# Kernel tuning notes

Measured on AMD Instinct MI355X. Metric: run time of the kernel, lower is better.

The kernel has to match this reference:

```python
import jax, jax.numpy as jnp
import numpy as np

N, E, T, D, C = 20000, 160000, 3, 128, 128  # nodes, edges, replicas, in=out feat dim, num_classes
NUM_EDGES = 128  # linear1 output width (must be <= C for the H scatter to be in-range)


def setup_inputs() -> dict:
    key = jax.random.key(0)
    ks = jax.random.split(key, 8)
    s = 1.0 / np.sqrt(D)
    return {
        "edge_index": jax.random.randint(ks[0], (2, E), 0, N, dtype=jnp.int32),
        "features": jax.random.normal(ks[1], (N, D), jnp.float32),
        "lin_W": jax.random.normal(ks[2], (T, D, D), jnp.float32) * s,   # t per-replica Linears
        "lin_b": jnp.zeros((T, D), jnp.float32),
        "gcn1_W": jax.random.normal(ks[3], (D, C), jnp.float32) * s,
        "gcn1_b": jnp.zeros((C,), jnp.float32),
        "gcn2_W": jax.random.normal(ks[4], (C, C), jnp.float32) * s,
        "gcn2_b": jnp.zeros((C,), jnp.float32),
        "lin1_W": jax.random.normal(ks[5], (C, NUM_EDGES), jnp.float32) * s,
        "lin1_b": jnp.zeros((NUM_EDGES,), jnp.float32),
    }


def _gcn(x, W, b, src, dst, n):
    """PyG GCNConv: add self-loops, symmetric deg^-1/2 normalization, scatter-add."""
    loop = jnp.arange(n, dtype=src.dtype)
    src = jnp.concatenate([src, loop])
    dst = jnp.concatenate([dst, loop])
    deg = jax.ops.segment_sum(jnp.ones(src.shape, x.dtype), dst, num_segments=n)
    dinv = jax.lax.rsqrt(deg)  # deg >= 1 because of self-loops
    norm = dinv[src] * dinv[dst]
    xw = x @ W
    return jax.ops.segment_sum(xw[src] * norm[:, None], dst, num_segments=n) + b


def reference(edge_index, features, lin_W, lin_b, gcn1_W, gcn1_b, gcn2_W, gcn2_b, lin1_W, lin1_b):
    src, dst = edge_index[0], edge_index[1]
    n = features.shape[0]
    t = lin_W.shape[0]
    scale = features.shape[1] ** -0.5  # out_features ** -0.5
    # t linear replicas, concatenated along nodes -> [t*n, D]
    transformed = (jnp.einsum('nd,tde->tne', features, lin_W) + lin_b[:, None, :]).reshape(t * n, -1)
    # replicate-selection via cosine similarity (exact torch index order:
    # src.repeat_interleave(t) vs dst.repeat(t))
    rep_src = jnp.repeat(src, t)
    exp_dst = jnp.tile(dst, t)
    a = features[rep_src]
    bb = transformed[exp_dst]
    sim = (a * bb).sum(-1) / jnp.maximum(
        jnp.linalg.norm(a, axis=-1) * jnp.linalg.norm(bb, axis=-1), 1e-8)
    best = jnp.argmax(sim.reshape(-1, t), axis=1)            # [E]
    best_nodes = dst + best.astype(dst.dtype) * n            # index into replica blocks
    # extra edges: (arange(n), arange(n) + i*n) for i in range(t)
    extra_src = jnp.tile(jnp.arange(n, dtype=src.dtype), t)
    extra_dst = (jnp.arange(n, dtype=src.dtype)[None, :]
                 + (jnp.arange(t, dtype=src.dtype) * n)[:, None]).reshape(-1)
    src_all = jnp.concatenate([src, src, extra_src])
    dst_all = jnp.concatenate([dst, best_nodes, extra_dst])
    nt = (t + 1) * n
    all_features = jnp.concatenate([features, transformed], axis=0)  # [(t+1)n, D]
    # GCN backbone (dropout = identity in eval mode)
    h = jax.nn.relu(all_features)
    h = jax.nn.relu(_gcn(h, gcn1_W, gcn1_b, src_all, dst_all, nt))
    all_features2 = _gcn(h, gcn2_W, gcn2_b, src_all, dst_all, nt)    # [(t+1)n, C]
    logits = jax.nn.relu(all_features2) @ lin1_W + lin1_b            # [(t+1)n, NUM_EDGES]
    num_classes = gcn2_b.shape[0]
    classes = jnp.argmax(logits.reshape(t + 1, n, -1), axis=-1)      # [t+1, n]
    H = jax.nn.one_hot(classes, num_classes, dtype=features.dtype).sum(0)  # [n, C] vote counts
    # per-class segment sum over nodes with H[:, j] > 0 (only first n rows are ever selected)
    mask = (H > 0).astype(features.dtype)                            # [n, C]
    hyperedge_features = mask.T @ all_features2[:n]                  # [C, D]
    dots = (all_features @ hyperedge_features.T) * scale             # [(t+1)n, C]
    H = jax.nn.softmax(H, axis=0)
    return H, hyperedge_features, dots
```

## Files before the change

kernel.cpp:

```cpp
#include <hip/hip_runtime.h>
#include <math.h>

#define NN 20000
#define NE 160000
#define TT 3
#define DD 128
#define NTOT 80000
#define N3 60000
#define NBLK1 79
#define SIMW 20000

__device__ __forceinline__ float waveReduceSum(float v) {
#pragma unroll
  for (int off = 32; off >= 1; off >>= 1)
    v += __shfl_xor(v, off, 64);
  return v;
}

__device__ __forceinline__ void atomAddF(float* p, float v) {
  unsafeAtomicAdd(p, v);
}

__global__ __launch_bounds__(256) void k_copy_feat(const float* __restrict__ src,
                                                   float* __restrict__ dst, int n4) {
  int i = blockIdx.x * 256 + threadIdx.x;
  if (i < n4) ((float4*)dst)[i] = ((const float4*)src)[i];
}

template <int RELU_IN, int TRANS_W, int DO_ARGMAX>
__global__ __launch_bounds__(512, 3) void gemm128(const float* __restrict__ X,
                                                  const float* __restrict__ W,
                                                  const float* __restrict__ bias,
                                                  float* __restrict__ out, int M,
                                                  float scale, int wStride, int bStride,
                                                  long oStride, int* __restrict__ cls) {
  __shared__ float Ws[128 * 132];
  const int tid = threadIdx.x;
  const int rbase = blockIdx.x * 160;
  W += (long)blockIdx.y * wStride;
  if (bias) bias += (long)blockIdx.y * bStride;
  out += (long)blockIdx.y * oStride;

#pragma unroll
  for (int it = 0; it < 8; ++it) {
    int idx = (tid + it * 512) * 4;
    int kl = idx >> 7, c = idx & 127;
    float4 w;
    if (!TRANS_W) {
      w = *(const float4*)&W[kl * 128 + c];
    } else {
      w.x = W[(c + 0) * 128 + kl];
      w.y = W[(c + 1) * 128 + kl];
      w.z = W[(c + 2) * 128 + kl];
      w.w = W[(c + 3) * 128 + kl];
    }
    *(float4*)&Ws[kl * 132 + c] = w;
  }

  const int tc = tid & 15, tr = tid >> 4;
  const int c0a = tc * 4, c0b = 64 + tc * 4;
  const int r0 = tr * 5;

  const float4* xrow[5];
#pragma unroll
  for (int i = 0; i < 5; ++i) {
    int gr = rbase + r0 + i;
    int gc = (gr < M) ? gr : 0;
    xrow[i] = (const float4*)(X + (long)gc * 128);
  }

  float acc[5][8];
#pragma unroll
  for (int i = 0; i < 5; ++i)
#pragma unroll
    for (int j = 0; j < 8; ++j) acc[i][j] = 0.f;

  float4 xc[5], xn[5];
#pragma unroll
  for (int i = 0; i < 5; ++i) {
    float4 v = xrow[i][0];
    if (RELU_IN) {
      v.x = fmaxf(v.x, 0.f);
      v.y = fmaxf(v.y, 0.f);
      v.z = fmaxf(v.z, 0.f);
      v.w = fmaxf(v.w, 0.f);
    }
    xc[i] = v;
  }

  __syncthreads();

  for (int kq = 0; kq < 32; ++kq) {
    if (kq < 31) {
#pragma unroll
      for (int i = 0; i < 5; ++i) {
        float4 v = xrow[i][kq + 1];
        if (RELU_IN) {
          v.x = fmaxf(v.x, 0.f);
          v.y = fmaxf(v.y, 0.f);
          v.z = fmaxf(v.z, 0.f);
          v.w = fmaxf(v.w, 0.f);
        }
        xn[i] = v;
      }
    }
    const int klb = kq * 4;
#pragma unroll
    for (int k = 0; k < 4; ++k) {
      const int kl = klb + k;
      const float4 wa = *(const float4*)&Ws[kl * 132 + c0a];
      const float4 wb = *(const float4*)&Ws[kl * 132 + c0b];
      float av[5];
#pragma unroll
      for (int i = 0; i < 5; ++i)
        av[i] = (k == 0) ? xc[i].x : (k == 1) ? xc[i].y : (k == 2) ? xc[i].z : xc[i].w;
      const float bv[8] = {wa.x, wa.y, wa.z, wa.w, wb.x, wb.y, wb.z, wb.w};
#pragma unroll
      for (int i = 0; i < 5; ++i)
#pragma unroll
        for (int j = 0; j < 8; ++j) acc[i][j] = fmaf(av[i], bv[j], acc[i][j]);
    }
    if (kq < 31) {
#pragma unroll
      for (int i = 0; i < 5; ++i) xc[i] = xn[i];
    }
  }

  float bb[8];
#pragma unroll
  for (int j = 0; j < 8; ++j) bb[j] = 0.f;
  if (bias) {
#pragma unroll
    for (int j = 0; j < 4; ++j) bb[j] = bias[c0a + j];
#pragma unroll
    for (int j = 0; j < 4; ++j) bb[4 + j] = bias[c0b + j];
  }

  if (DO_ARGMAX) {
#pragma unroll
    for (int i = 0; i < 5; ++i) {
      float bv = acc[i][0] * scale + bb[0];
      int bc = c0a;
#pragma unroll
      for (int j = 1; j < 8; ++j) {
        float v = acc[i][j] * scale + bb[j];
        int col = (j < 4) ? (c0a + j) : (c0b + j - 4);
        if (v > bv) {
          bv = v;
          bc = col;
        }
      }
#pragma unroll
      for (int off = 1; off <= 8; off <<= 1) {
        float ov = __shfl_xor(bv, off, 64);
        int oc = __shfl_xor(bc, off, 64);
        if (ov > bv || (ov == bv && oc < bc)) {
          bv = ov;
          bc = oc;
        }
      }
      int gr = rbase + r0 + i;
      if (tc == 0 && gr < M) cls[gr] = bc;
    }
  } else {
#pragma unroll
    for (int i = 0; i < 5; ++i) {
      int gr = rbase + r0 + i;
      if (gr < M) {
        float4 v0, v1;
        v0.x = acc[i][0] * scale + bb[0];
        v0.y = acc[i][1] * scale + bb[1];
        v0.z = acc[i][2] * scale + bb[2];
        v0.w = acc[i][3] * scale + bb[3];
        v1.x = acc[i][4] * scale + bb[4];
        v1.y = acc[i][5] * scale + bb[5];
        v1.z = acc[i][6] * scale + bb[6];
        v1.w = acc[i][7] * scale + bb[7];
        *(float4*)&out[(long)gr * 128 + c0a] = v0;
        *(float4*)&out[(long)gr * 128 + c0b] = v1;
      }
    }
  }
}

__global__ __launch_bounds__(256) void k_norms(const float* __restrict__ feat,
                                               const float* __restrict__ A,
                                               float* __restrict__ nf,
                                               float* __restrict__ nt0) {
  int w = blockIdx.x * 4 + (threadIdx.x >> 6);
  int lane = threadIdx.x & 63;
  if (w >= 2 * NN) return;
  const float* p = (w < NN) ? (feat + (long)w * 128) : (A + (long)(NN + (w - NN)) * 128);
  float2 v = *(const float2*)(p + lane * 2);
  float s = waveReduceSum(v.x * v.x + v.y * v.y);
  if (lane == 0) {
    float r = sqrtf(s);
    if (w < NN) nf[w] = r;
    else nt0[w - NN] = r;
  }
}

__global__ __launch_bounds__(256) void k_sim(const int* __restrict__ ei,
                                             const float* __restrict__ feat,
                                             const float* __restrict__ A,
                                             const float* __restrict__ nf,
                                             const float* __restrict__ nt0,
                                             int* __restrict__ bn) {
  const int t = threadIdx.x;
  const int lane = t & 31;
  const int half = (t >> 5) & 1;
  const int w = blockIdx.x * 4 + (t >> 6);

#define SIM_LOAD(I, E, DE, AV, B0, B1, B2, NA, NB0, NB1, NB2)              \
  {                                                                        \
    E = 2 * (w + (I)*SIMW) + half;                                         \
    DE = ei[NE + E];                                                       \
    int s_ = ei[E];                                                        \
    int j0_ = 3 * E;                                                       \
    if (j0_ >= NE) j0_ -= NE;                                              \
    if (j0_ >= NE) j0_ -= NE;                                              \
    int j1_ = j0_ + 1;                                                     \
    if (j1_ >= NE) j1_ -= NE;                                              \
    int j2_ = j0_ + 2;                                                     \
    if (j2_ >= NE) j2_ -= NE;                                              \
    int d0_ = ei[NE + j0_], d1_ = ei[NE + j1_], d2_ = ei[NE + j2_];        \
    AV = ((const float4*)(feat + (long)s_ * 128))[lane];                   \
    B0 = ((const float4*)(A + (long)(NN + d0_) * 128))[lane];              \
    B1 = ((const float4*)(A + (long)(NN + d1_) * 128))[lane];              \
    B2 = ((const float4*)(A + (long)(NN + d2_) * 128))[lane];              \
    NA = nf[s_];                                                           \
    NB0 = nt0[d0_];                                                        \
    NB1 = nt0[d1_];                                                        \
    NB2 = nt0[d2_];                                                        \
  }

  int ec, dec;
  float4 ac, b0c, b1c, b2c;
  float nac, nb0c, nb1c, nb2c;
  SIM_LOAD(0, ec, dec, ac, b0c, b1c, b2c, nac, nb0c, nb1c, nb2c);

#pragma unroll
  for (int i = 0; i < 4; ++i) {
    int en = 0, den = 0;
    float4 an, b0n, b1n, b2n;
    float nan2 = 0.f, nb0n = 0.f, nb1n = 0.f, nb2n = 0.f;
    if (i < 3) {
      SIM_LOAD(i + 1, en, den, an, b0n, b1n, b2n, nan2, nb0n, nb1n, nb2n);
    }
    float p0 = ac.x * b0c.x + ac.y * b0c.y + ac.z * b0c.z + ac.w * b0c.w;
    float p1 = ac.x * b1c.x + ac.y * b1c.y + ac.z * b1c.z + ac.w * b1c.w;
    float p2 = ac.x * b2c.x + ac.y * b2c.y + ac.z * b2c.z + ac.w * b2c.w;
#pragma unroll
    for (int off = 1; off <= 16; off <<= 1) {
      p0 += __shfl_xor(p0, off, 64);
      p1 += __shfl_xor(p1, off, 64);
      p2 += __shfl_xor(p2, off, 64);
    }
    float s0 = p0 / fmaxf(nac * nb0c, 1e-8f);
    float s1 = p1 / fmaxf(nac * nb1c, 1e-8f);
    float s2 = p2 / fmaxf(nac * nb2c, 1e-8f);
    int bk = 0;
    float bv = s0;
    if (s1 > bv) {
      bv = s1;
      bk = 1;
    }
    if (s2 > bv) {
      bv = s2;
      bk = 2;
    }
    if (lane == 0) bn[ec] = dec + bk * NN;
    if (i < 3) {
      ec = en;
      dec = den;
      ac = an;
      b0c = b0n;
      b1c = b1n;
      b2c = b2n;
      nac = nan2;
      nb0c = nb0n;
      nb1c = nb1n;
      nb2c = nb2n;
    }
  }
#undef SIM_LOAD
}

__global__ __launch_bounds__(256) void k_zero_count(int* __restrict__ count) {
  int v = blockIdx.x * 256 + threadIdx.x;
  if (v < NTOT) count[v] = 0;
}

__global__ __launch_bounds__(256) void k_count(const int* __restrict__ ei,
                                               const int* __restrict__ bn,
                                               int* __restrict__ count) {
  int e = blockIdx.x * 256 + threadIdx.x;
  if (e < NE) {
    atomicAdd(&count[ei[NE + e]], 1);
    atomicAdd(&count[bn[e]], 1);
  }
}

__global__ __launch_bounds__(256) void k_dinv(const int* __restrict__ count,
                                              float* __restrict__ dinv) {
  int v = blockIdx.x * 256 + threadIdx.x;
  if (v < NTOT) {
    float deg = (float)count[v] + ((v < N3) ? 2.f : 1.f);
    dinv[v] = 1.f / sqrtf(deg);
  }
}

__global__ __launch_bounds__(256) void k_scan1(const int* __restrict__ count,
                                               int* __restrict__ start,
                                               int* __restrict__ bsum) {
  __shared__ int sh[256];
  const int b = blockIdx.x, t = threadIdx.x;
  const int base = b * 1024 + t * 4;
  int c[4];
  int s = 0;
#pragma unroll
  for (int k = 0; k < 4; ++k) {
    int idx = base + k;
    c[k] = (idx < NTOT) ? count[idx] : 0;
    s += c[k];
  }
  sh[t] = s;
  __syncthreads();
  for (int off = 1; off < 256; off <<= 1) {
    int v = (t >= off) ? sh[t - off] : 0;
    __syncthreads();
    sh[t] += v;
    __syncthreads();
  }
  if (t == 255) bsum[b] = sh[255];
  int run = sh[t] - s;
#pragma unroll
  for (int k = 0; k < 4; ++k) {
    int idx = base + k;
    if (idx < NTOT) start[idx] = run;
    run += c[k];
  }
}

__global__ __launch_bounds__(256) void k_scan2(int* __restrict__ bsum) {
  __shared__ int sh[256];
  const int t = threadIdx.x;
  int v = (t < NBLK1) ? bsum[t] : 0;
  sh[t] = v;
  __syncthreads();
  for (int off = 1; off < 256; off <<= 1) {
    int u = (t >= off) ? sh[t - off] : 0;
    __syncthreads();
    sh[t] += u;
    __syncthreads();
  }
  if (t < NBLK1) bsum[t] = sh[t] - v;
}

__global__ __launch_bounds__(256) void k_scan3(int* __restrict__ start,
                                               const int* __restrict__ bsum,
                                               int* __restrict__ cursor) {
  int i = blockIdx.x * 256 + threadIdx.x;
  if (i < NTOT) {
    int v = start[i] + bsum[i >> 10];
    start[i] = v;
    cursor[i] = v;
  }
}

__global__ __launch_bounds__(256) void k_fill(const int* __restrict__ ei,
                                              const int* __restrict__ bn,
                                              const float* __restrict__ dinv,
                                              int* __restrict__ cursor,
                                              int2* __restrict__ ent) {
  int g = blockIdx.x * 256 + threadIdx.x;
  if (g >= 2 * NE) return;
  int e = (g < NE) ? g : g - NE;
  int s = ei[e];
  int d = (g < NE) ? ei[NE + e] : bn[e];
  float w = dinv[s] * dinv[d];
  int pos = atomicAdd(&cursor[d], 1);
  ent[pos] = make_int2(s, __float_as_int(w));
}

__global__ __launch_bounds__(256) void k_agg(const int2* __restrict__ ent,
                                             const int* __restrict__ start,
                                             const int* __restrict__ end,
                                             const float* __restrict__ xw,
                                             const float* __restrict__ dinv,
                                             const float* __restrict__ bias,
                                             float* __restrict__ out) {
  const int t = threadIdx.x;
  const int lane = t & 31;
  const int v = blockIdx.x * 8 + (t >> 5);
  float dv = dinv[v];
  float4 xv = ((const float4*)(xw + (long)v * 128))[lane];
  float4 bb = ((const float4*)bias)[lane];
  float a0 = bb.x + dv * dv * xv.x;
  float a1 = bb.y + dv * dv * xv.y;
  float a2 = bb.z + dv * dv * xv.z;
  float a3 = bb.w + dv * dv * xv.w;
  if (v < NN) {
    a0 += dv * dv * xv.x;
    a1 += dv * dv * xv.y;
    a2 += dv * dv * xv.z;
    a3 += dv * dv * xv.w;
  } else if (v < N3) {
    int j = (v < 2 * NN) ? v - NN : v - 2 * NN;
    float4 xj = ((const float4*)(xw + (long)j * 128))[lane];
    float w = dinv[j] * dv;
    a0 = fmaf(w, xj.x, a0);
    a1 = fmaf(w, xj.y, a1);
    a2 = fmaf(w, xj.z, a2);
    a3 = fmaf(w, xj.w, a3);
  }
  int i = start[v];
  const int i1 = end[v];
  if (i < i1) {
    int2 e0 = ent[i];
    float4 x0 = ((const float4*)(xw + (long)e0.x * 128))[lane];
    for (; i + 1 < i1; ++i) {
      int2 e1 = ent[i + 1];
      float4 x1 = ((const float4*)(xw + (long)e1.x * 128))[lane];
      float w0 = __int_as_float(e0.y);
      a0 = fmaf(w0, x0.x, a0);
      a1 = fmaf(w0, x0.y, a1);
      a2 = fmaf(w0, x0.z, a2);
      a3 = fmaf(w0, x0.w, a3);
      e0 = e1;
      x0 = x1;
    }
    float w0 = __int_as_float(e0.y);
    a0 = fmaf(w0, x0.x, a0);
    a1 = fmaf(w0, x0.y, a1);
    a2 = fmaf(w0, x0.z, a2);
    a3 = fmaf(w0, x0.w, a3);
  }
  ((float4*)(out + (long)v * 128))[lane] = make_float4(a0, a1, a2, a3);
}

__global__ __launch_bounds__(256) void k_zero_small(float* __restrict__ hyper,
                                                    int* __restrict__ hist) {
  int i = blockIdx.x * 256 + threadIdx.x;
  if (i < 128 * 128) hyper[i] = 0.f;
  if (i < 640) hist[i] = 0;
}

#define HISTBLK 20
__global__ __launch_bounds__(256) void k_hist(const int* __restrict__ cls,
                                              int* __restrict__ hist) {
  __shared__ int sh[640];
  const int t = threadIdx.x;
  for (int i = t; i < 640; i += 256) sh[i] = 0;
  __syncthreads();
  const int per = NN / HISTBLK;
  const int j0 = blockIdx.x * per;
  for (int j = j0 + t; j < j0 + per; j += 256) {
    int cc[4] = {cls[j], cls[NN + j], cls[2 * NN + j], cls[3 * NN + j]};
#pragma unroll
    for (int i = 0; i < 4; ++i) {
      bool first = true;
      int m = 0;
#pragma unroll
      for (int k = 0; k < 4; ++k) {
        if (cc[k] == cc[i]) {
          if (k < i) first = false;
          m++;
        }
      }
      if (first) atomicAdd(&sh[cc[i] * 5 + m], 1);
    }
  }
  __syncthreads();
  for (int i = t; i < 640; i += 256) {
    int v = sh[i];
    if (v) atomicAdd(&hist[i], v);
  }
}

__global__ void k_table(const int* __restrict__ hist, float* __restrict__ table) {
  int c = threadIdx.x;
  if (c >= 128) return;
  int cnt[5];
  int tot = 0;
  for (int v = 1; v <= 4; ++v) {
    cnt[v] = hist[c * 5 + v];
    tot += cnt[v];
  }
  cnt[0] = NN - tot;
  int m = 0;
  for (int v = 0; v <= 4; ++v)
    if (cnt[v] > 0) m = v;
  float ex[5];
  float denom = 0.f;
  for (int v = 0; v <= 4; ++v) {
    ex[v] = expf((float)(v - m));
    denom += (float)cnt[v] * ex[v];
  }
  for (int v = 0; v <= 4; ++v) table[c * 5 + v] = ex[v] / denom;
}

__global__ __launch_bounds__(256) void k_hwrite(const int* __restrict__ cls,
                                                const float* __restrict__ table,
                                                float* __restrict__ H) {
  int j = blockIdx.x * 2 + (threadIdx.x >> 7);
  int c = threadIdx.x & 127;
  if (j >= NN) return;
  int c0 = cls[j], c1 = cls[NN + j], c2 = cls[2 * NN + j], c3 = cls[3 * NN + j];
  int cnt = (c == c0) + (c == c1) + (c == c2) + (c == c3);
  H[(long)j * 128 + c] = table[c * 5 + cnt];
}

#define HBLK 250
#define HPER 80
__global__ __launch_bounds__(256) void k_hyper(const int* __restrict__ cls,
                                               const float* __restrict__ af2,
                                               float* __restrict__ hyper) {
  __shared__ float acc[128 * 128];
  const int t = threadIdx.x;
  for (int i = t; i < 128 * 128; i += 256) acc[i] = 0.f;
  __syncthreads();
  const int j0 = blockIdx.x * HPER;
  const int j1 = j0 + HPER;
  const int d = t & 127;
  const int half = t >> 7;
  float v = af2[(long)j0 * 128 + d];
  int c0 = cls[j0], c1 = cls[NN + j0], c2 = cls[2 * NN + j0], c3 = cls[3 * NN + j0];
  for (int j = j0; j < j1; ++j) {
    float vn = 0.f;
    int n0 = 0, n1 = 0, n2 = 0, n3 = 0;
    if (j + 1 < j1) {
      vn = af2[(long)(j + 1) * 128 + d];
      n0 = cls[j + 1];
      n1 = cls[NN + j + 1];
      n2 = cls[2 * NN + j + 1];
      n3 = cls[3 * NN + j + 1];
    }
    if (half == 0) {
      atomicAdd(&acc[c0 * 128 + d], v);
      if (c2 != c0 && c2 != c1) atomicAdd(&acc[c2 * 128 + d], v);
    } else {
      if (c1 != c0) atomicAdd(&acc[c1 * 128 + d], v);
      if (c3 != c0 && c3 != c1 && c3 != c2) atomicAdd(&acc[c3 * 128 + d], v);
    }
    v = vn;
    c0 = n0;
    c1 = n1;
    c2 = n2;
    c3 = n3;
  }
  __syncthreads();
  for (int i = t; i < 128 * 128; i += 256) {
    float x = acc[i];
    if (x != 0.f) atomAddF(&hyper[i], x);
  }
}

extern "C" void kernel_launch(void* const* d_in, const int* in_sizes, int n_in,
                              void* d_out, int out_size, void* d_ws, size_t ws_size,
                              hipStream_t stream) {
  (void)in_sizes;
  (void)n_in;
  (void)out_size;
  (void)ws_size;
  const int* ei = (const int*)d_in[0];
  const float* feat = (const float*)d_in[1];
  const float* lin_W = (const float*)d_in[2];
  const float* lin_b = (const float*)d_in[3];
  const float* g1W = (const float*)d_in[4];
  const float* g1b = (const float*)d_in[5];
  const float* g2W = (const float*)d_in[6];
  const float* g2b = (const float*)d_in[7];
  const float* l1W = (const float*)d_in[8];
  const float* l1b = (const float*)d_in[9];

  float* out = (float*)d_out;
  float* H = out;
  float* hyper = out + (size_t)NN * 128;
  float* dots = hyper + 128 * 128;

  float* ws = (float*)d_ws;
  float* A = ws;
  float* Cb = A + (size_t)NTOT * 128;
  float* Bb = dots;
  float* dinv = Cb + (size_t)NTOT * 128;
  float* nf = dinv + NTOT;
  float* nt0 = nf + NN;
  int* bn = (int*)(nt0 + NN);
  int* cls = bn + NE;
  int* hist = cls + NTOT;
  float* table = (float*)(hist + 640);
  int* count = (int*)(table + 640);
  int* startA = count + NTOT;
  int* cursor = startA + NTOT;
  int* bsum = cursor + NTOT;
  int2* ent = (int2*)(bsum + 128);

  const float kScale = 0.08838834764831843f;

  k_copy_feat<<<(NN * 128 / 4 + 255) / 256, 256, 0, stream>>>(feat, A, NN * 128 / 4);
  gemm128<0, 0, 0><<<dim3(125, 3), 512, 0, stream>>>(
      feat, lin_W, lin_b, A + (size_t)NN * 128, NN, 1.f, 128 * 128, 128,
      (long)NN * 128, nullptr);
  k_norms<<<10000, 256, 0, stream>>>(feat, A, nf, nt0);
  k_zero_count<<<(NTOT + 255) / 256, 256, 0, stream>>>(count);
  k_sim<<<SIMW / 4, 256, 0, stream>>>(ei, feat, A, nf, nt0, bn);
  k_count<<<(NE + 255) / 256, 256, 0, stream>>>(ei, bn, count);
  k_dinv<<<(NTOT + 255) / 256, 256, 0, stream>>>(count, dinv);
  k_scan1<<<NBLK1, 256, 0, stream>>>(count, startA, bsum);
  k_scan2<<<1, 256, 0, stream>>>(bsum);
  k_scan3<<<(NTOT + 255) / 256, 256, 0, stream>>>(startA, bsum, cursor);
  k_fill<<<(2 * NE + 255) / 256, 256, 0, stream>>>(ei, bn, dinv, cursor, ent);
  gemm128<1, 0, 0><<<dim3(NTOT / 160, 1), 512, 0, stream>>>(A, g1W, nullptr, Bb, NTOT,
                                                            1.f, 0, 0, 0, nullptr);
  k_agg<<<NTOT / 8, 256, 0, stream>>>(ent, startA, cursor, Bb, dinv, g1b, Cb);
  gemm128<1, 0, 0><<<dim3(NTOT / 160, 1), 512, 0, stream>>>(Cb, g2W, nullptr, Bb, NTOT,
                                                            1.f, 0, 0, 0, nullptr);
  k_agg<<<NTOT / 8, 256, 0, stream>>>(ent, startA, cursor, Bb, dinv, g2b, Cb);
  gemm128<1, 0, 1><<<dim3(NTOT / 160, 1), 512, 0, stream>>>(Cb, l1W, l1b, nullptr,
                                                            NTOT, 1.f, 0, 0, 0, cls);
  k_zero_small<<<64, 256, 0, stream>>>(hyper, hist);
  k_hist<<<HISTBLK, 256, 0, stream>>>(cls, hist);
  k_table<<<1, 128, 0, stream>>>(hist, table);
  k_hwrite<<<NN / 2, 256, 0, stream>>>(cls, table, H);
  k_hyper<<<HBLK, 256, 0, stream>>>(cls, Cb, hyper);
  gemm128<0, 1, 0><<<dim3(NTOT / 160, 1), 512, 0, stream>>>(A, hyper, nullptr, dots,
                                                            NTOT, kScale, 0, 0, 0,
                                                            nullptr);
}
```

Baseline: 417.6 us.

## Fold feature copy, dinv, and block-sum scan into neighboring kernels

Removes three small kernel launches. The feature copy into the workspace moves into k_norms, which already reads those rows. The dinv array is dropped and each consumer recomputes it from the degree count. The block-sum scan is redone inside every k_scan3 block. This trades launch overhead and one pass over global memory for extra per-block scan work and repeated rsqrt math inside k_fill and k_agg.

```diff
diff --git a/kernel.cpp b/kernel.cpp
--- a/kernel.cpp
+++ b/kernel.cpp
@@ -21,10 +21,9 @@
   unsafeAtomicAdd(p, v);
 }
 
-__global__ __launch_bounds__(256) void k_copy_feat(const float* __restrict__ src,
-                                                   float* __restrict__ dst, int n4) {
-  int i = blockIdx.x * 256 + threadIdx.x;
-  if (i < n4) ((float4*)dst)[i] = ((const float4*)src)[i];
+__device__ __forceinline__ float dinvOf(const int* __restrict__ count, int v) {
+  float deg = (float)count[v] + ((v < N3) ? 2.f : 1.f);
+  return 1.f / sqrtf(deg);
 }
 
 template <int RELU_IN, int TRANS_W, int DO_ARGMAX>
@@ -184,14 +183,19 @@
 }
 
 __global__ __launch_bounds__(256) void k_norms(const float* __restrict__ feat,
-                                               const float* __restrict__ A,
+                                               float* __restrict__ A,
                                                float* __restrict__ nf,
                                                float* __restrict__ nt0) {
   int w = blockIdx.x * 4 + (threadIdx.x >> 6);
   int lane = threadIdx.x & 63;
   if (w >= 2 * NN) return;
-  const float* p = (w < NN) ? (feat + (long)w * 128) : (A + (long)(NN + (w - NN)) * 128);
-  float2 v = *(const float2*)(p + lane * 2);
+  float2 v;
+  if (w < NN) {
+    v = *(const float2*)(feat + (long)w * 128 + lane * 2);
+    *(float2*)(A + (long)w * 128 + lane * 2) = v;
+  } else {
+    v = *(const float2*)(A + (long)(NN + (w - NN)) * 128 + lane * 2);
+  }
   float s = waveReduceSum(v.x * v.x + v.y * v.y);
   if (lane == 0) {
     float r = sqrtf(s);
@@ -301,15 +305,6 @@
   }
 }
 
-__global__ __launch_bounds__(256) void k_dinv(const int* __restrict__ count,
-                                              float* __restrict__ dinv) {
-  int v = blockIdx.x * 256 + threadIdx.x;
-  if (v < NTOT) {
-    float deg = (float)count[v] + ((v < N3) ? 2.f : 1.f);
-    dinv[v] = 1.f / sqrtf(deg);
-  }
-}
-
 __global__ __launch_bounds__(256) void k_scan1(const int* __restrict__ count,
                                                int* __restrict__ start,
                                                int* __restrict__ bsum) {
@@ -342,27 +337,28 @@
   }
 }
 
-__global__ __launch_bounds__(256) void k_scan2(int* __restrict__ bsum) {
-  __shared__ int sh[256];
-  const int t = threadIdx.x;
-  int v = (t < NBLK1) ? bsum[t] : 0;
-  sh[t] = v;
-  __syncthreads();
-  for (int off = 1; off < 256; off <<= 1) {
-    int u = (t >= off) ? sh[t - off] : 0;
-    __syncthreads();
-    sh[t] += u;
-    __syncthreads();
-  }
-  if (t < NBLK1) bsum[t] = sh[t] - v;
-}
-
 __global__ __launch_bounds__(256) void k_scan3(int* __restrict__ start,
                                                const int* __restrict__ bsum,
                                                int* __restrict__ cursor) {
-  int i = blockIdx.x * 256 + threadIdx.x;
+  __shared__ int sh[128];
+  const int t = threadIdx.x;
+  int mine = 0;
+  if (t < 128) {
+    mine = (t < NBLK1) ? bsum[t] : 0;
+    sh[t] = mine;
+  }
+  __syncthreads();
+  for (int off = 1; off < 128; off <<= 1) {
+    int u = (t < 128 && t >= off) ? sh[t - off] : 0;
+    __syncthreads();
+    if (t < 128) sh[t] += u;
+    __syncthreads();
+  }
+  int i = blockIdx.x * 256 + t;
   if (i < NTOT) {
-    int v = start[i] + bsum[i >> 10];
+    int g = i >> 10;
+    int excl = sh[g] - bsum[g];
+    int v = start[i] + excl;
     start[i] = v;
     cursor[i] = v;
   }
@@ -370,7 +366,7 @@
 
 __global__ __launch_bounds__(256) void k_fill(const int* __restrict__ ei,
                                               const int* __restrict__ bn,
-                                              const float* __restrict__ dinv,
+                                              const int* __restrict__ count,
                                               int* __restrict__ cursor,
                                               int2* __restrict__ ent) {
   int g = blockIdx.x * 256 + threadIdx.x;
@@ -378,7 +374,7 @@
   int e = (g < NE) ? g : g - NE;
   int s = ei[e];
   int d = (g < NE) ? ei[NE + e] : bn[e];
-  float w = dinv[s] * dinv[d];
+  float w = dinvOf(count, s) * dinvOf(count, d);
   int pos = atomicAdd(&cursor[d], 1);
   ent[pos] = make_int2(s, __float_as_int(w));
 }
@@ -387,13 +383,13 @@
                                              const int* __restrict__ start,
                                              const int* __restrict__ end,
                                              const float* __restrict__ xw,
-                                             const float* __restrict__ dinv,
+                                             const int* __restrict__ count,
                                              const float* __restrict__ bias,
                                              float* __restrict__ out) {
   const int t = threadIdx.x;
   const int lane = t & 31;
   const int v = blockIdx.x * 8 + (t >> 5);
-  float dv = dinv[v];
+  float dv = dinvOf(count, v);
   float4 xv = ((const float4*)(xw + (long)v * 128))[lane];
   float4 bb = ((const float4*)bias)[lane];
   float a0 = bb.x + dv * dv * xv.x;
@@ -408,7 +404,7 @@
   } else if (v < N3) {
     int j = (v < 2 * NN) ? v - NN : v - 2 * NN;
     float4 xj = ((const float4*)(xw + (long)j * 128))[lane];
-    float w = dinv[j] * dv;
+    float w = dinvOf(count, j) * dv;
     a0 = fmaf(w, xj.x, a0);
     a1 = fmaf(w, xj.y, a1);
     a2 = fmaf(w, xj.z, a2);
@@ -583,8 +579,7 @@
   float* A = ws;
   float* Cb = A + (size_t)NTOT * 128;
   float* Bb = dots;
-  float* dinv = Cb + (size_t)NTOT * 128;
-  float* nf = dinv + NTOT;
+  float* nf = Cb + (size_t)NTOT * 128;
   float* nt0 = nf + NN;
   int* bn = (int*)(nt0 + NN);
   int* cls = bn + NE;
@@ -598,7 +593,6 @@
 
   const float kScale = 0.08838834764831843f;
 
-  k_copy_feat<<<(NN * 128 / 4 + 255) / 256, 256, 0, stream>>>(feat, A, NN * 128 / 4);
   gemm128<0, 0, 0><<<dim3(125, 3), 512, 0, stream>>>(
       feat, lin_W, lin_b, A + (size_t)NN * 128, NN, 1.f, 128 * 128, 128,
       (long)NN * 128, nullptr);
@@ -606,17 +600,15 @@
   k_zero_count<<<(NTOT + 255) / 256, 256, 0, stream>>>(count);
   k_sim<<<SIMW / 4, 256, 0, stream>>>(ei, feat, A, nf, nt0, bn);
   k_count<<<(NE + 255) / 256, 256, 0, stream>>>(ei, bn, count);
-  k_dinv<<<(NTOT + 255) / 256, 256, 0, stream>>>(count, dinv);
   k_scan1<<<NBLK1, 256, 0, stream>>>(count, startA, bsum);
-  k_scan2<<<1, 256, 0, stream>>>(bsum);
   k_scan3<<<(NTOT + 255) / 256, 256, 0, stream>>>(startA, bsum, cursor);
-  k_fill<<<(2 * NE + 255) / 256, 256, 0, stream>>>(ei, bn, dinv, cursor, ent);
+  k_fill<<<(2 * NE + 255) / 256, 256, 0, stream>>>(ei, bn, count, cursor, ent);
   gemm128<1, 0, 0><<<dim3(NTOT / 160, 1), 512, 0, stream>>>(A, g1W, nullptr, Bb, NTOT,
                                                             1.f, 0, 0, 0, nullptr);
-  k_agg<<<NTOT / 8, 256, 0, stream>>>(ent, startA, cursor, Bb, dinv, g1b, Cb);
+  k_agg<<<NTOT / 8, 256, 0, stream>>>(ent, startA, cursor, Bb, count, g1b, Cb);
   gemm128<1, 0, 0><<<dim3(NTOT / 160, 1), 512, 0, stream>>>(Cb, g2W, nullptr, Bb, NTOT,
                                                             1.f, 0, 0, 0, nullptr);
-  k_agg<<<NTOT / 8, 256, 0, stream>>>(ent, startA, cursor, Bb, dinv, g2b, Cb);
+  k_agg<<<NTOT / 8, 256, 0, stream>>>(ent, startA, cursor, Bb, count, g2b, Cb);
   gemm128<1, 0, 1><<<dim3(NTOT / 160, 1), 512, 0, stream>>>(Cb, l1W, l1b, nullptr,
                                                             NTOT, 1.f, 0, 0, 0, cls);
   k_zero_small<<<64, 256, 0, stream>>>(hyper, hist);
```

Result: no change. 414.4 us (-0.8%).
